# Kernel tuning notes

Measured on AMD Instinct MI355X. Metric: run time of the kernel, lower is better.

Reference implementation:

```python
import jax, jax.numpy as jnp
import numpy as np

B, S, DIM = 2, 2048, 2048
NH, NKV, HD = 32, 8, 64
N_REP = NH // NKV


def apply_rope(x, cos, sin):
    # x: (B, H, S, HD); cos/sin: (S, HD//2)
    d = x.shape[-1] // 2
    x1, x2 = x[..., :d], x[..., d:]
    c = cos[None, None, :, :]
    s = sin[None, None, :, :]
    return jnp.concatenate([x1 * c - x2 * s, x2 * c + x1 * s], axis=-1)


def setup_inputs() -> dict:
    key = jax.random.key(0)
    ks = jax.random.split(key, 8)
    x = jax.random.normal(ks[0], (B, S, DIM), dtype=jnp.float32)
    # plausible RoPE tables
    inv_freq = 1.0 / (10000.0 ** (jnp.arange(0, HD, 2, dtype=jnp.float32) / HD))
    t = jnp.arange(S, dtype=jnp.float32)
    freqs = jnp.outer(t, inv_freq)  # (S, HD//2)
    rope_cos = jnp.cos(freqs)
    rope_sin = jnp.sin(freqs)
    doc_ids = jnp.sort(jax.random.randint(ks[1], (B, S), 0, 8, dtype=jnp.int32), axis=-1)
    std = 0.02
    Wq = jax.random.normal(ks[2], (NH * HD, DIM), dtype=jnp.float32) * std
    Wk = jax.random.normal(ks[3], (NKV * HD, DIM), dtype=jnp.float32) * std
    Wv = jax.random.normal(ks[4], (NKV * HD, DIM), dtype=jnp.float32) * std
    Wo = jax.random.normal(ks[5], (DIM, NH * HD), dtype=jnp.float32) * std
    return {"x": x, "rope_cos": rope_cos, "rope_sin": rope_sin,
            "doc_ids": doc_ids, "Wq": Wq, "Wk": Wk, "Wv": Wv, "Wo": Wo}


def reference(x, rope_cos, rope_sin, doc_ids, Wq, Wk, Wv, Wo):
    batch, seq_len, _ = x.shape
    q = (x @ Wq.T).reshape(batch, seq_len, NH, HD).transpose(0, 2, 1, 3)   # (B,NH,S,HD)
    k = (x @ Wk.T).reshape(batch, seq_len, NKV, HD).transpose(0, 2, 1, 3)  # (B,NKV,S,HD)
    v = (x @ Wv.T).reshape(batch, seq_len, NKV, HD).transpose(0, 2, 1, 3)

    q = apply_rope(q, rope_cos, rope_sin)
    k = apply_rope(k, rope_cos, rope_sin)

    # GQA expansion (repeat_interleave on head dim)
    k = jnp.repeat(k, N_REP, axis=1)  # (B,NH,S,HD)
    v = jnp.repeat(v, N_REP, axis=1)

    # block-diagonal causal mask from packed doc ids
    doc_mask = doc_ids[:, :, None] == doc_ids[:, None, :]          # (B,S,S)
    causal = jnp.tril(jnp.ones((seq_len, seq_len), dtype=bool))    # (S,S)
    mask = (doc_mask & causal[None])[:, None, :, :]                # (B,1,S,S)

    scale = 1.0 / jnp.sqrt(jnp.asarray(HD, dtype=q.dtype))
    scores = jnp.einsum("bhqd,bhkd->bhqk", q, k) * scale
    scores = jnp.where(mask, scores, jnp.finfo(scores.dtype).min)
    attn = jax.nn.softmax(scores, axis=-1)
    out = jnp.einsum("bhqk,bhkd->bhqd", attn, v)                   # (B,NH,S,HD)
    out = out.transpose(0, 2, 1, 3).reshape(batch, seq_len, NH * HD)
    return out @ Wo.T
```

## Files before the change

### kernel.cpp

```cpp
#include <hip/hip_runtime.h>
#include <hip/hip_bf16.h>

#define BB   2
#define SEQ  2048
#define DIMD 2048
#define NHH  32
#define NKVV 8
#define HDD  64
#define QKVS 3072

typedef __bf16 bf16x8 __attribute__((ext_vector_type(8)));
typedef float  floatx4 __attribute__((ext_vector_type(4)));

typedef __attribute__((address_space(1))) const void* gas_ptr;
typedef __attribute__((address_space(3))) void*       las_ptr;

__device__ __forceinline__ unsigned short f2bu(float f) {
    __hip_bfloat16 h = __float2bfloat16(f);
    return *reinterpret_cast<unsigned short*>(&h);
}

#define C_X  (8u  * 1024 * 1024)
#define C_WQ (4u  * 1024 * 1024)
#define C_WK (1u  * 1024 * 1024)
#define C_WV (1u  * 1024 * 1024)
#define C_WO (4u  * 1024 * 1024)
__global__ void cvt_all(const float* __restrict__ x,  const float* __restrict__ wq,
                        const float* __restrict__ wk, const float* __restrict__ wv,
                        const float* __restrict__ wo,
                        __hip_bfloat16* __restrict__ xb,
                        __hip_bfloat16* __restrict__ wqkv,
                        __hip_bfloat16* __restrict__ wob)
{
    unsigned i = (blockIdx.x * blockDim.x + threadIdx.x) * 4;
    const float* src; __hip_bfloat16* dst;
    if (i < C_X)                       { src = x  + i;                    dst = xb + i; }
    else if (i < C_X + C_WQ)           { unsigned o = i - C_X;            src = wq + o; dst = wqkv + o; }
    else if (i < C_X + C_WQ + C_WK)    { unsigned o = i - C_X - C_WQ;     src = wk + o; dst = wqkv + C_WQ + o; }
    else if (i < C_X + C_WQ + C_WK + C_WV) { unsigned o = i - C_X - C_WQ - C_WK; src = wv + o; dst = wqkv + C_WQ + C_WK + o; }
    else                               { unsigned o = i - C_X - C_WQ - C_WK - C_WV; if (o >= C_WO) return; src = wo + o; dst = wob + o; }
    float4 v = *reinterpret_cast<const float4*>(src);
    dst[0] = __float2bfloat16(v.x);
    dst[1] = __float2bfloat16(v.y);
    dst[2] = __float2bfloat16(v.z);
    dst[3] = __float2bfloat16(v.w);
}

template <typename OutT, bool ROPE>
__global__ __launch_bounds__(256) void gemm_lds(
    const __hip_bfloat16* __restrict__ Abf,
    const __hip_bfloat16* __restrict__ Wbf,
    OutT* __restrict__ C,
    int M, int N, int K, int ldc,
    const float* __restrict__ cosb, const float* __restrict__ sinb)
{
    const __bf16* A = reinterpret_cast<const __bf16*>(Abf);
    const __bf16* W = reinterpret_cast<const __bf16*>(Wbf);

    __shared__ __bf16 As[128 * 32];
    __shared__ __bf16 Bs[128 * 32];

    int tid  = threadIdx.x;
    int wid  = tid >> 6;
    int lane = tid & 63;
    int l15  = lane & 15;
    int l4   = lane >> 4;
    int wm   = (wid & 1) * 64;
    int wn   = (wid >> 1) * 64;
    int bm   = blockIdx.x * 128;
    int bn   = blockIdx.y * 128;

    int r0 = tid >> 2,         g0 = (tid & 3) ^ ((r0 >> 1) & 3);
    int r1 = (tid + 256) >> 2, g1 = (tid & 3) ^ ((r1 >> 1) & 3);

    const __bf16* a0 = A + (size_t)(bm + r0) * K + g0 * 8;
    const __bf16* a1 = A + (size_t)(bm + r1) * K + g1 * 8;
    const __bf16* w0 = W + (size_t)(bn + r0) * K + g0 * 8;
    const __bf16* w1 = W + (size_t)(bn + r1) * K + g1 * 8;

    __bf16* lA0 = As + tid * 8;
    __bf16* lA1 = As + (tid + 256) * 8;
    __bf16* lB0 = Bs + tid * 8;
    __bf16* lB1 = Bs + (tid + 256) * 8;

    int arow[4], aslot[4], brow[4], bslot[4];
    #pragma unroll
    for (int i = 0; i < 4; ++i) {
        int ra = wm + i * 16 + l15;
        int rb = wn + i * 16 + l15;
        arow[i] = ra; aslot[i] = l4 ^ ((ra >> 1) & 3);
        brow[i] = rb; bslot[i] = l4 ^ ((rb >> 1) & 3);
    }

    floatx4 acc[4][4] = {};

    for (int k0 = 0; k0 < K; k0 += 32) {
        __builtin_amdgcn_global_load_lds((gas_ptr)(a0 + k0), (las_ptr)lA0, 16, 0, 0);
        __builtin_amdgcn_global_load_lds((gas_ptr)(a1 + k0), (las_ptr)lA1, 16, 0, 0);
        __builtin_amdgcn_global_load_lds((gas_ptr)(w0 + k0), (las_ptr)lB0, 16, 0, 0);
        __builtin_amdgcn_global_load_lds((gas_ptr)(w1 + k0), (las_ptr)lB1, 16, 0, 0);
        __syncthreads();

        bf16x8 af[4], bfr[4];
        #pragma unroll
        for (int i = 0; i < 4; ++i)
            af[i] = *reinterpret_cast<const bf16x8*>(As + arow[i] * 32 + aslot[i] * 8);
        #pragma unroll
        for (int j = 0; j < 4; ++j)
            bfr[j] = *reinterpret_cast<const bf16x8*>(Bs + brow[j] * 32 + bslot[j] * 8);

        #pragma unroll
        for (int i = 0; i < 4; ++i)
            #pragma unroll
            for (int j = 0; j < 4; ++j)
                acc[i][j] = __builtin_amdgcn_mfma_f32_16x16x32_bf16(af[i], bfr[j], acc[i][j], 0, 0, 0);
        __syncthreads();
    }

    if constexpr (ROPE) {
        bool do_rope = (bn + wn) < 2560;
        #pragma unroll
        for (int i = 0; i < 4; ++i) {
            #pragma unroll
            for (int r = 0; r < 4; ++r) {
                int row = bm + wm + i * 16 + l4 * 4 + r;
                int s   = row & (SEQ - 1);
                #pragma unroll
                for (int j = 0; j < 2; ++j) {
                    float x1 = acc[i][j][r], x2 = acc[i][j + 2][r];
                    if (do_rope) {
                        float cf = cosb[s * 32 + j * 16 + l15];
                        float sf = sinb[s * 32 + j * 16 + l15];
                        float o1 = x1 * cf - x2 * sf;
                        float o2 = x2 * cf + x1 * sf;
                        x1 = o1; x2 = o2;
                    }
                    int col = bn + wn + j * 16 + l15;
                    C[(size_t)row * ldc + col]      = __float2bfloat16(x1);
                    C[(size_t)row * ldc + col + 32] = __float2bfloat16(x2);
                }
            }
        }
    } else {
        #pragma unroll
        for (int i = 0; i < 4; ++i)
            #pragma unroll
            for (int j = 0; j < 4; ++j)
                #pragma unroll
                for (int r = 0; r < 4; ++r) {
                    int row = bm + wm + i * 16 + l4 * 4 + r;
                    int col = bn + wn + j * 16 + l15;
                    if constexpr (sizeof(OutT) == 4)
                        C[(size_t)row * ldc + col] = acc[i][j][r];
                    else
                        C[(size_t)row * ldc + col] = __float2bfloat16(acc[i][j][r]);
                }
    }
}

__global__ void transpose_v(const __hip_bfloat16* __restrict__ qkv,
                            unsigned short* __restrict__ vT)
{
    __shared__ unsigned short T[64][68];
    int s0  = blockIdx.x * 64;
    int kvh = blockIdx.y;
    int b   = blockIdx.z;
    int tid = threadIdx.x;

    int srow = tid >> 2, dg = (tid & 3) * 16;
    const unsigned short* src = reinterpret_cast<const unsigned short*>(qkv)
        + (size_t)(b * SEQ + s0 + srow) * QKVS + 2560 + kvh * 64 + dg;
    #pragma unroll
    for (int i = 0; i < 4; ++i)
        *reinterpret_cast<ushort4*>(&T[srow][dg + i * 4]) =
            *reinterpret_cast<const ushort4*>(src + i * 4);
    __syncthreads();

    int drow = tid >> 2, sg = (tid & 3) * 16;
    unsigned short* dst = vT + ((size_t)(b * NKVV + kvh) * 64 + drow) * SEQ + s0 + sg;
    #pragma unroll
    for (int i = 0; i < 4; ++i) {
        ushort4 u;
        u.x = T[sg + i * 4 + 0][drow];
        u.y = T[sg + i * 4 + 1][drow];
        u.z = T[sg + i * 4 + 2][drow];
        u.w = T[sg + i * 4 + 3][drow];
        *reinterpret_cast<ushort4*>(dst + i * 4) = u;
    }
}

__global__ __launch_bounds__(256) void attn_mfma(
    const __hip_bfloat16* __restrict__ qkv,
    const unsigned short* __restrict__ vT,
    const int* __restrict__ doc,
    __hip_bfloat16* __restrict__ ob)
{
    int qblk = (int)gridDim.x - 1 - (int)blockIdx.x;
    int h    = blockIdx.y;
    int b    = blockIdx.z;
    int kvh  = h >> 2;
    int tid  = threadIdx.x;
    int wv   = tid >> 6;
    int lane = tid & 63;
    int l15  = lane & 15;
    int l4   = lane >> 4;
    int q0   = qblk * 128;
    int qw   = q0 + wv * 32;

    __shared__ unsigned short Ks[64 * 64];
    __shared__ unsigned short Vts[64 * 64];
    __shared__ unsigned short Pb[4][32][76];
    __shared__ int kdoc[64];

    const unsigned short* qus = reinterpret_cast<const unsigned short*>(qkv);
    const unsigned short* kus = qus + 2048;

    bf16x8 aq[2][2];
    #pragma unroll
    for (int qt = 0; qt < 2; ++qt) {
        const unsigned short* qrow = qus + (size_t)(b * SEQ + qw + qt * 16 + l15) * QKVS + h * HDD;
        aq[qt][0] = *reinterpret_cast<const bf16x8*>(qrow + l4 * 8);
        aq[qt][1] = *reinterpret_cast<const bf16x8*>(qrow + 32 + l4 * 8);
    }
    int qd[2][4];
    #pragma unroll
    for (int qt = 0; qt < 2; ++qt)
        #pragma unroll
        for (int r = 0; r < 4; ++r)
            qd[qt][r] = doc[b * SEQ + qw + qt * 16 + l4 * 4 + r];
    int qd_w   = doc[b * SEQ + qw];
    int qd_blk = doc[b * SEQ + q0];

    float mrow[2][4], lrow[2][4];
    #pragma unroll
    for (int qt = 0; qt < 2; ++qt)
        #pragma unroll
        for (int r = 0; r < 4; ++r) { mrow[qt][r] = -1e30f; lrow[qt][r] = 0.f; }
    floatx4 accO[2][4] = {};

    int slot0 = tid, slot1 = tid + 256;
    int row0 = slot0 >> 3, g0 = (slot0 & 7) ^ (row0 & 7);
    int row1 = slot1 >> 3, g1 = (slot1 & 7) ^ (row1 & 7);
    const unsigned short* vtb = vT + ((size_t)(b * NKVV + kvh) * 64) * SEQ;

    int kc_end = 2 * qblk + 1;
    for (int kc = 0; kc <= kc_end; ++kc) {
        int k0 = kc * 64;
        int kd_last = doc[b * SEQ + k0 + 63];
        if (kd_last < qd_blk) continue;

        __syncthreads();
        __builtin_amdgcn_global_load_lds(
            (gas_ptr)(kus + (size_t)(b * SEQ + k0 + row0) * QKVS + kvh * HDD + g0 * 8),
            (las_ptr)(Ks + slot0 * 8), 16, 0, 0);
        __builtin_amdgcn_global_load_lds(
            (gas_ptr)(kus + (size_t)(b * SEQ + k0 + row1) * QKVS + kvh * HDD + g1 * 8),
            (las_ptr)(Ks + slot1 * 8), 16, 0, 0);
        __builtin_amdgcn_global_load_lds(
            (gas_ptr)(vtb + (size_t)row0 * SEQ + k0 + g0 * 8),
            (las_ptr)(Vts + slot0 * 8), 16, 0, 0);
        __builtin_amdgcn_global_load_lds(
            (gas_ptr)(vtb + (size_t)row1 * SEQ + k0 + g1 * 8),
            (las_ptr)(Vts + slot1 * 8), 16, 0, 0);
        if (tid < 64) kdoc[tid] = doc[b * SEQ + k0 + tid];
        __syncthreads();

        if (k0 <= qw + 31 && kd_last >= qd_w) {
            #pragma unroll
            for (int qt = 0; qt < 2; ++qt) {
                float s[4][4];
                #pragma unroll
                for (int t = 0; t < 4; ++t) {
                    int krow = t * 16 + l15;
                    bf16x8 bk0 = *reinterpret_cast<const bf16x8*>(Ks + krow * 64 + ((l4 ^ (krow & 7)) * 8));
                    bf16x8 bk1 = *reinterpret_cast<const bf16x8*>(Ks + krow * 64 + ((((l4 + 4)) ^ (krow & 7)) * 8));
                    floatx4 acc = {};
                    acc = __builtin_amdgcn_mfma_f32_16x16x32_bf16(aq[qt][0], bk0, acc, 0, 0, 0);
                    acc = __builtin_amdgcn_mfma_f32_16x16x32_bf16(aq[qt][1], bk1, acc, 0, 0, 0);
                    int key = k0 + krow;
                    int kd  = kdoc[krow];
                    #pragma unroll
                    for (int r = 0; r < 4; ++r) {
                        int qrow = qw + qt * 16 + l4 * 4 + r;
                        bool valid = (kd == qd[qt][r]) && (key <= qrow);
                        s[t][r] = valid ? acc[r] * 0.125f : -1e30f;
                    }
                }
                #pragma unroll
                for (int r = 0; r < 4; ++r) {
                    float pm = fmaxf(fmaxf(s[0][r], s[1][r]), fmaxf(s[2][r], s[3][r]));
                    pm = fmaxf(pm, __shfl_xor(pm, 1));
                    pm = fmaxf(pm, __shfl_xor(pm, 2));
                    pm = fmaxf(pm, __shfl_xor(pm, 4));
                    pm = fmaxf(pm, __shfl_xor(pm, 8));
                    float mnew = fmaxf(mrow[qt][r], pm);
                    float alpha = __expf(mrow[qt][r] - mnew);
                    mrow[qt][r] = mnew;
                    float ps = 0.f;
                    #pragma unroll
                    for (int t = 0; t < 4; ++t) {
                        float p = (s[t][r] <= -1e29f) ? 0.f : __expf(s[t][r] - mnew);
                        Pb[wv][qt * 16 + l4 * 4 + r][t * 16 + l15] = f2bu(p);
                        ps += p;
                    }
                    ps += __shfl_xor(ps, 1);
                    ps += __shfl_xor(ps, 2);
                    ps += __shfl_xor(ps, 4);
                    ps += __shfl_xor(ps, 8);
                    lrow[qt][r] = lrow[qt][r] * alpha + ps;
                    #pragma unroll
                    for (int t = 0; t < 4; ++t) accO[qt][t][r] *= alpha;
                }
            }
            #pragma unroll
            for (int qt = 0; qt < 2; ++qt) {
                bf16x8 ap0 = *reinterpret_cast<const bf16x8*>(&Pb[wv][qt * 16 + l15][l4 * 8]);
                bf16x8 ap1 = *reinterpret_cast<const bf16x8*>(&Pb[wv][qt * 16 + l15][32 + l4 * 8]);
                #pragma unroll
                for (int t = 0; t < 4; ++t) {
                    int vrow = t * 16 + l15;
                    bf16x8 bv0 = *reinterpret_cast<const bf16x8*>(Vts + vrow * 64 + ((l4 ^ (vrow & 7)) * 8));
                    bf16x8 bv1 = *reinterpret_cast<const bf16x8*>(Vts + vrow * 64 + ((((l4 + 4)) ^ (vrow & 7)) * 8));
                    accO[qt][t] = __builtin_amdgcn_mfma_f32_16x16x32_bf16(ap0, bv0, accO[qt][t], 0, 0, 0);
                    accO[qt][t] = __builtin_amdgcn_mfma_f32_16x16x32_bf16(ap1, bv1, accO[qt][t], 0, 0, 0);
                }
            }
        }
    }

    #pragma unroll
    for (int qt = 0; qt < 2; ++qt)
        #pragma unroll
        for (int r = 0; r < 4; ++r) {
            float inv = 1.0f / lrow[qt][r];
            size_t base = (size_t)(b * SEQ + qw + qt * 16 + l4 * 4 + r) * (NHH * HDD) + h * HDD;
            #pragma unroll
            for (int t = 0; t < 4; ++t)
                ob[base + t * 16 + l15] = __float2bfloat16(accO[qt][t][r] * inv);
        }
}

extern "C" void kernel_launch(void* const* d_in, const int* in_sizes, int n_in,
                              void* d_out, int out_size, void* d_ws, size_t ws_size,
                              hipStream_t stream) {
    const float* x  = (const float*)d_in[0];
    const float* rc = (const float*)d_in[1];
    const float* rs = (const float*)d_in[2];
    const int*   dc = (const int*)d_in[3];
    const float* Wq = (const float*)d_in[4];
    const float* Wk = (const float*)d_in[5];
    const float* Wv = (const float*)d_in[6];
    const float* Wo = (const float*)d_in[7];
    float* out = (float*)d_out;

    const int M   = BB * SEQ;
    const int KVD = NKVV * HDD;
    const int QKVN = DIMD + 2 * KVD;

    char* ws = (char*)d_ws;
    size_t off = 0;
    auto alloc = [&](size_t elems) { __hip_bfloat16* p = (__hip_bfloat16*)(ws + off); off += elems * 2; return p; };
    __hip_bfloat16* xb   = alloc((size_t)M * DIMD);
    __hip_bfloat16* wqkv = alloc((size_t)QKVN * DIMD);
    __hip_bfloat16* wob  = alloc((size_t)DIMD * DIMD);
    __hip_bfloat16* qkv  = alloc((size_t)M * QKVN);
    __hip_bfloat16* abuf = alloc((size_t)M * DIMD);
    unsigned short* vtb  = (unsigned short*)alloc((size_t)BB * NKVV * HDD * SEQ);

    {
        unsigned total4 = (C_X + C_WQ + C_WK + C_WV + C_WO) / 4;
        cvt_all<<<dim3((total4 + 255) / 256), 256, 0, stream>>>(
            x, Wq, Wk, Wv, Wo, xb, wqkv, wob);
    }

    gemm_lds<__hip_bfloat16, true><<<dim3(M / 128, QKVN / 128), 256, 0, stream>>>(
        xb, wqkv, qkv, M, QKVN, DIMD, QKVN, rc, rs);

    transpose_v<<<dim3(SEQ / 64, NKVV, BB), 256, 0, stream>>>(qkv, vtb);

    attn_mfma<<<dim3(SEQ / 128, NHH, BB), 256, 0, stream>>>(qkv, vtb, dc, abuf);

    gemm_lds<float, false><<<dim3(M / 128, DIMD / 128), 256, 0, stream>>>(
        abuf, wob, out, M, DIMD, DIMD, DIMD, nullptr, nullptr);
}
```

Baseline: 304.7 us.

## Replace GEMM with 8-wave double-buffered 256-row tile kernel with interleaved staging

Replaces the simple 128x128 single-buffer GEMM with a 512-thread kernel that computes 256xBN tiles (BN=256 for the QKV projection, 128 for the output projection), using K-tiles of 64 and double-buffered LDS. Global-to-LDS loads for the next tile are interleaved with MFMA phases, with explicit barriers, waitcnt and setprio. A remapped 1D grid groups workgroups for better cache locality. The aim is to hide memory latency and raise data reuse per tile. In exchange it uses much more LDS, fewer and larger workgroups, and fragile hand scheduling whose correctness depends on the waitcnt counts.

```diff
diff --git a/kernel.cpp b/kernel.cpp
--- a/kernel.cpp
+++ b/kernel.cpp
@@ -14,6 +14,9 @@
 
 typedef __attribute__((address_space(1))) const void* gas_ptr;
 typedef __attribute__((address_space(3))) void*       las_ptr;
+
+#define MFMA16 __builtin_amdgcn_mfma_f32_16x16x32_bf16
+#define CBAR() asm volatile("" ::: "memory")
 
 __device__ __forceinline__ unsigned short f2bu(float f) {
     __hip_bfloat16 h = __float2bfloat16(f);
@@ -46,88 +49,161 @@
     dst[3] = __float2bfloat16(v.w);
 }
 
-template <typename OutT, bool ROPE>
-__global__ __launch_bounds__(256) void gemm_lds(
+template <typename OutT, bool ROPE, int BN>
+__global__ __launch_bounds__(512, 2) void gemm8p(
     const __hip_bfloat16* __restrict__ Abf,
     const __hip_bfloat16* __restrict__ Wbf,
     OutT* __restrict__ C,
     int M, int N, int K, int ldc,
     const float* __restrict__ cosb, const float* __restrict__ sinb)
 {
-    const __bf16* A = reinterpret_cast<const __bf16*>(Abf);
-    const __bf16* W = reinterpret_cast<const __bf16*>(Wbf);
-
-    __shared__ __bf16 As[128 * 32];
-    __shared__ __bf16 Bs[128 * 32];
-
-    int tid  = threadIdx.x;
-    int wid  = tid >> 6;
-    int lane = tid & 63;
-    int l15  = lane & 15;
-    int l4   = lane >> 4;
-    int wm   = (wid & 1) * 64;
-    int wn   = (wid >> 1) * 64;
-    int bm   = blockIdx.x * 128;
-    int bn   = blockIdx.y * 128;
-
-    int r0 = tid >> 2,         g0 = (tid & 3) ^ ((r0 >> 1) & 3);
-    int r1 = (tid + 256) >> 2, g1 = (tid & 3) ^ ((r1 >> 1) & 3);
-
-    const __bf16* a0 = A + (size_t)(bm + r0) * K + g0 * 8;
-    const __bf16* a1 = A + (size_t)(bm + r1) * K + g1 * 8;
-    const __bf16* w0 = W + (size_t)(bn + r0) * K + g0 * 8;
-    const __bf16* w1 = W + (size_t)(bn + r1) * K + g1 * 8;
-
-    __bf16* lA0 = As + tid * 8;
-    __bf16* lA1 = As + (tid + 256) * 8;
-    __bf16* lB0 = Bs + tid * 8;
-    __bf16* lB1 = Bs + (tid + 256) * 8;
-
-    int arow[4], aslot[4], brow[4], bslot[4];
-    #pragma unroll
-    for (int i = 0; i < 4; ++i) {
-        int ra = wm + i * 16 + l15;
-        int rb = wn + i * 16 + l15;
-        arow[i] = ra; aslot[i] = l4 ^ ((ra >> 1) & 3);
-        brow[i] = rb; bslot[i] = l4 ^ ((rb >> 1) & 3);
-    }
-
-    floatx4 acc[4][4] = {};
-
-    for (int k0 = 0; k0 < K; k0 += 32) {
-        __builtin_amdgcn_global_load_lds((gas_ptr)(a0 + k0), (las_ptr)lA0, 16, 0, 0);
-        __builtin_amdgcn_global_load_lds((gas_ptr)(a1 + k0), (las_ptr)lA1, 16, 0, 0);
-        __builtin_amdgcn_global_load_lds((gas_ptr)(w0 + k0), (las_ptr)lB0, 16, 0, 0);
-        __builtin_amdgcn_global_load_lds((gas_ptr)(w1 + k0), (las_ptr)lB1, 16, 0, 0);
-        __syncthreads();
-
-        bf16x8 af[4], bfr[4];
-        #pragma unroll
-        for (int i = 0; i < 4; ++i)
-            af[i] = *reinterpret_cast<const bf16x8*>(As + arow[i] * 32 + aslot[i] * 8);
-        #pragma unroll
-        for (int j = 0; j < 4; ++j)
-            bfr[j] = *reinterpret_cast<const bf16x8*>(Bs + brow[j] * 32 + bslot[j] * 8);
-
-        #pragma unroll
-        for (int i = 0; i < 4; ++i)
-            #pragma unroll
-            for (int j = 0; j < 4; ++j)
-                acc[i][j] = __builtin_amdgcn_mfma_f32_16x16x32_bf16(af[i], bfr[j], acc[i][j], 0, 0, 0);
-        __syncthreads();
+    constexpr int  NF = BN / 64;
+    constexpr int  WN = BN / 4;
+    constexpr bool B2 = (BN == 256);
+    constexpr int  HB = (BN / 2) * 64;
+
+    const __bf16* Ag = reinterpret_cast<const __bf16*>(Abf);
+    const __bf16* Wg = reinterpret_cast<const __bf16*>(Wbf);
+
+    __shared__ __align__(16) __bf16 As[2][256 * 64];
+    __shared__ __align__(16) __bf16 Bs[2][BN * 64];
+
+    const int NT   = K >> 6;
+    const int tid  = threadIdx.x;
+    const int wid  = tid >> 6;
+    const int lane = tid & 63;
+    const int l15  = lane & 15;
+    const int l4   = lane >> 4;
+    const int wm   = wid >> 2;
+    const int wn   = wid & 3;
+
+    const int gx   = M >> 8;
+    const int nwg  = (int)gridDim.x;
+    const int orig = (int)blockIdx.x;
+    const int wg   = (orig & 7) * (nwg >> 3) + (orig >> 3);
+    const int bm   = (wg % gx) << 8;
+    const int bn   = (wg / gx) * BN;
+
+    const int r0 = tid >> 3;
+    const int c0 = ((tid & 7) ^ (r0 & 7)) * 8;
+    const __bf16* aS00 = Ag + (size_t)(bm + r0) * K + c0;
+    const __bf16* aS01 = aS00 + (size_t)64  * K;
+    const __bf16* aS10 = aS00 + (size_t)128 * K;
+    const __bf16* aS11 = aS00 + (size_t)192 * K;
+    const __bf16* bS00 = Wg + (size_t)(bn + r0) * K + c0;
+    const __bf16* bS01 = bS00 + (size_t)64 * K;
+    const __bf16* bS10 = bS00 + (size_t)(BN / 2) * K;
+    const __bf16* bS11 = bS10 + (size_t)64 * K;
+
+    bf16x8 af[4][2], b01[2][2], b23[2][2];
+    floatx4 acc[8][NF] = {};
+
+    auto stage2 = [&](const __bf16* s0, const __bf16* s1, __bf16* d, int kt) {
+        int k0 = (kt < NT ? kt : NT - 1) << 6;
+        __builtin_amdgcn_global_load_lds((gas_ptr)(s0 + k0), (las_ptr)(d + tid * 8), 16, 0, 0);
+        if (s1)
+        __builtin_amdgcn_global_load_lds((gas_ptr)(s1 + k0), (las_ptr)(d + 4096 + tid * 8), 16, 0, 0);
+    };
+    auto lda = [&](int buf, int mbase) {
+        #pragma unroll
+        for (int mi = 0; mi < 4; ++mi)
+            #pragma unroll
+            for (int kk = 0; kk < 2; ++kk) {
+                int row = wm * 128 + (mbase + mi) * 16 + l15;
+                int ch  = ((kk * 4 + l4) ^ (row & 7)) * 8;
+                af[mi][kk] = *reinterpret_cast<const bf16x8*>(&As[buf][row * 64 + ch]);
+            }
+    };
+    auto ldb = [&](int buf, bf16x8 (&regs)[2][2], int nbase) {
+        #pragma unroll
+        for (int ni = 0; ni < 2; ++ni)
+            #pragma unroll
+            for (int kk = 0; kk < 2; ++kk) {
+                int row = wn * WN + (nbase + ni) * 16 + l15;
+                int ch  = ((kk * 4 + l4) ^ (row & 7)) * 8;
+                regs[ni][kk] = *reinterpret_cast<const bf16x8*>(&Bs[buf][row * 64 + ch]);
+            }
+    };
+    auto mmBoth = [&](int mbase, bf16x8 (&bregs)[2][2], int nb) {
+        #pragma unroll
+        for (int mi = 0; mi < 4; ++mi)
+            #pragma unroll
+            for (int ni = 0; ni < 2; ++ni) {
+                acc[mbase + mi][nb + ni] = MFMA16(af[mi][0], bregs[ni][0], acc[mbase + mi][nb + ni], 0, 0, 0);
+                acc[mbase + mi][nb + ni] = MFMA16(af[mi][1], bregs[ni][1], acc[mbase + mi][nb + ni], 0, 0, 0);
+            }
+    };
+    auto mmOne = [&](int mbase, int kk) {
+        #pragma unroll
+        for (int mi = 0; mi < 4; ++mi)
+            #pragma unroll
+            for (int ni = 0; ni < 2; ++ni)
+                acc[mbase + mi][ni] = MFMA16(af[mi][kk], b01[ni][kk], acc[mbase + mi][ni], 0, 0, 0);
+    };
+
+    auto ktile = [&](int cur, int t) {
+        lda(cur, 0);
+        ldb(cur, b01, 0);
+        stage2(aS10, aS11, &As[cur ^ 1][8192], t + 1);
+        CBAR(); __builtin_amdgcn_s_barrier(); CBAR();
+        asm volatile("s_waitcnt lgkmcnt(0)" ::: "memory");
+        __builtin_amdgcn_sched_barrier(0);
+        __builtin_amdgcn_s_setprio(1);
+        if constexpr (B2) mmBoth(0, b01, 0); else mmOne(0, 0);
+        __builtin_amdgcn_s_setprio(0);
+        CBAR(); __builtin_amdgcn_s_barrier(); CBAR();
+        if constexpr (B2) ldb(cur, b23, 2);
+        stage2(bS00, B2 ? bS01 : (const __bf16*)nullptr, &Bs[cur ^ 1][0], t + 1);
+        CBAR(); __builtin_amdgcn_s_barrier(); CBAR();
+        asm volatile("s_waitcnt lgkmcnt(0)" ::: "memory");
+        __builtin_amdgcn_sched_barrier(0);
+        __builtin_amdgcn_s_setprio(1);
+        if constexpr (B2) mmBoth(0, b23, 2); else mmOne(0, 1);
+        __builtin_amdgcn_s_setprio(0);
+        CBAR(); __builtin_amdgcn_s_barrier(); CBAR();
+        lda(cur, 4);
+        stage2(bS10, B2 ? bS11 : (const __bf16*)nullptr, &Bs[cur ^ 1][HB], t + 1);
+        CBAR(); __builtin_amdgcn_s_barrier(); CBAR();
+        asm volatile("s_waitcnt lgkmcnt(0)" ::: "memory");
+        __builtin_amdgcn_sched_barrier(0);
+        __builtin_amdgcn_s_setprio(1);
+        if constexpr (B2) mmBoth(4, b23, 2); else mmOne(4, 1);
+        __builtin_amdgcn_s_setprio(0);
+        CBAR(); __builtin_amdgcn_s_barrier(); CBAR();
+        stage2(aS00, aS01, &As[cur][0], t + 2);
+        CBAR(); __builtin_amdgcn_s_barrier(); CBAR();
+        __builtin_amdgcn_s_setprio(1);
+        if constexpr (B2) mmBoth(4, b01, 0); else mmOne(4, 0);
+        __builtin_amdgcn_s_setprio(0);
+        asm volatile("s_waitcnt vmcnt(2)" ::: "memory");
+        CBAR(); __builtin_amdgcn_s_barrier(); CBAR();
+    };
+
+    stage2(aS00, aS01, &As[0][0],    0);
+    stage2(aS10, aS11, &As[0][8192], 0);
+    stage2(bS00, B2 ? bS01 : (const __bf16*)nullptr, &Bs[0][0],  0);
+    stage2(bS10, B2 ? bS11 : (const __bf16*)nullptr, &Bs[0][HB], 0);
+    stage2(aS00, aS01, &As[1][0],    1);
+    asm volatile("s_waitcnt vmcnt(2)" ::: "memory");
+    CBAR(); __builtin_amdgcn_s_barrier(); CBAR();
+
+    #pragma unroll 1
+    for (int t = 0; t < NT; t += 2) {
+        ktile(0, t);
+        ktile(1, t + 1);
     }
 
     if constexpr (ROPE) {
-        bool do_rope = (bn + wn) < 2560;
-        #pragma unroll
-        for (int i = 0; i < 4; ++i) {
+        bool do_rope = (bn + wn * 64) < 2560;
+        #pragma unroll
+        for (int mi = 0; mi < 8; ++mi) {
             #pragma unroll
             for (int r = 0; r < 4; ++r) {
-                int row = bm + wm + i * 16 + l4 * 4 + r;
+                int row = bm + wm * 128 + mi * 16 + l4 * 4 + r;
                 int s   = row & (SEQ - 1);
                 #pragma unroll
                 for (int j = 0; j < 2; ++j) {
-                    float x1 = acc[i][j][r], x2 = acc[i][j + 2][r];
+                    float x1 = acc[mi][j][r], x2 = acc[mi][j + 2][r];
                     if (do_rope) {
                         float cf = cosb[s * 32 + j * 16 + l15];
                         float sf = sinb[s * 32 + j * 16 + l15];
@@ -135,7 +211,7 @@
                         float o2 = x2 * cf + x1 * sf;
                         x1 = o1; x2 = o2;
                     }
-                    int col = bn + wn + j * 16 + l15;
+                    int col = bn + wn * 64 + j * 16 + l15;
                     C[(size_t)row * ldc + col]      = __float2bfloat16(x1);
                     C[(size_t)row * ldc + col + 32] = __float2bfloat16(x2);
                 }
@@ -143,17 +219,17 @@
         }
     } else {
         #pragma unroll
-        for (int i = 0; i < 4; ++i)
-            #pragma unroll
-            for (int j = 0; j < 4; ++j)
+        for (int mi = 0; mi < 8; ++mi)
+            #pragma unroll
+            for (int ni = 0; ni < NF; ++ni)
                 #pragma unroll
                 for (int r = 0; r < 4; ++r) {
-                    int row = bm + wm + i * 16 + l4 * 4 + r;
-                    int col = bn + wn + j * 16 + l15;
+                    int row = bm + wm * 128 + mi * 16 + l4 * 4 + r;
+                    int col = bn + wn * WN + ni * 16 + l15;
                     if constexpr (sizeof(OutT) == 4)
-                        C[(size_t)row * ldc + col] = acc[i][j][r];
+                        C[(size_t)row * ldc + col] = acc[mi][ni][r];
                     else
-                        C[(size_t)row * ldc + col] = __float2bfloat16(acc[i][j][r]);
+                        C[(size_t)row * ldc + col] = __float2bfloat16(acc[mi][ni][r]);
                 }
     }
 }
@@ -275,8 +351,8 @@
                     bf16x8 bk0 = *reinterpret_cast<const bf16x8*>(Ks + krow * 64 + ((l4 ^ (krow & 7)) * 8));
                     bf16x8 bk1 = *reinterpret_cast<const bf16x8*>(Ks + krow * 64 + ((((l4 + 4)) ^ (krow & 7)) * 8));
                     floatx4 acc = {};
-                    acc = __builtin_amdgcn_mfma_f32_16x16x32_bf16(aq[qt][0], bk0, acc, 0, 0, 0);
-                    acc = __builtin_amdgcn_mfma_f32_16x16x32_bf16(aq[qt][1], bk1, acc, 0, 0, 0);
+                    acc = MFMA16(aq[qt][0], bk0, acc, 0, 0, 0);
+                    acc = MFMA16(aq[qt][1], bk1, acc, 0, 0, 0);
                     int key = k0 + krow;
                     int kd  = kdoc[krow];
                     #pragma unroll
@@ -321,8 +397,8 @@
                     int vrow = t * 16 + l15;
                     bf16x8 bv0 = *reinterpret_cast<const bf16x8*>(Vts + vrow * 64 + ((l4 ^ (vrow & 7)) * 8));
                     bf16x8 bv1 = *reinterpret_cast<const bf16x8*>(Vts + vrow * 64 + ((((l4 + 4)) ^ (vrow & 7)) * 8));
-                    accO[qt][t] = __builtin_amdgcn_mfma_f32_16x16x32_bf16(ap0, bv0, accO[qt][t], 0, 0, 0);
-                    accO[qt][t] = __builtin_amdgcn_mfma_f32_16x16x32_bf16(ap1, bv1, accO[qt][t], 0, 0, 0);
+                    accO[qt][t] = MFMA16(ap0, bv0, accO[qt][t], 0, 0, 0);
+                    accO[qt][t] = MFMA16(ap1, bv1, accO[qt][t], 0, 0, 0);
                 }
             }
         }
@@ -353,8 +429,8 @@
     const float* Wo = (const float*)d_in[7];
     float* out = (float*)d_out;
 
-    const int M   = BB * SEQ;
-    const int KVD = NKVV * HDD;
+    const int M    = BB * SEQ;
+    const int KVD  = NKVV * HDD;
     const int QKVN = DIMD + 2 * KVD;
 
     char* ws = (char*)d_ws;
@@ -373,13 +449,13 @@
             x, Wq, Wk, Wv, Wo, xb, wqkv, wob);
     }
 
-    gemm_lds<__hip_bfloat16, true><<<dim3(M / 128, QKVN / 128), 256, 0, stream>>>(
+    gemm8p<__hip_bfloat16, true, 256><<<dim3((M / 256) * (QKVN / 256)), 512, 0, stream>>>(
         xb, wqkv, qkv, M, QKVN, DIMD, QKVN, rc, rs);
 
     transpose_v<<<dim3(SEQ / 64, NKVV, BB), 256, 0, stream>>>(qkv, vtb);
 
     attn_mfma<<<dim3(SEQ / 128, NHH, BB), 256, 0, stream>>>(qkv, vtb, dc, abuf);
 
-    gemm_lds<float, false><<<dim3(M / 128, DIMD / 128), 256, 0, stream>>>(
+    gemm8p<float, false, 128><<<dim3((M / 256) * (DIMD / 128)), 512, 0, stream>>>(
         abuf, wob, out, M, DIMD, DIMD, DIMD, nullptr, nullptr);
 }
```

Result: faster. 298.3 us (-2.1%).

## Fuse V transpose into QKV GEMM epilogue and double-buffer attention K/V tiles

Applied to the files above, without the earlier changes.

The QKV GEMM epilogue now writes V columns straight into the transposed V layout, which removes the separate transpose kernel and its extra read and write of V. The attention kernel precomputes a ballot mask of key chunks that can be relevant for the block, then double-buffers the K, V and doc-id tiles in LDS so the next chunk's loads overlap the current chunk's compute. Doc ids are also staged asynchronously. The risks are more LDS use, which may lower occupancy, and the correctness of the hand-written vmcnt waits.

```diff
diff --git a/kernel.cpp b/kernel.cpp
--- a/kernel.cpp
+++ b/kernel.cpp
@@ -14,6 +14,9 @@
 
 typedef __attribute__((address_space(1))) const void* gas_ptr;
 typedef __attribute__((address_space(3))) void*       las_ptr;
+
+#define MFMA16 __builtin_amdgcn_mfma_f32_16x16x32_bf16
+#define CBAR() asm volatile("" ::: "memory")
 
 __device__ __forceinline__ unsigned short f2bu(float f) {
     __hip_bfloat16 h = __float2bfloat16(f);
@@ -52,7 +55,8 @@
     const __hip_bfloat16* __restrict__ Wbf,
     OutT* __restrict__ C,
     int M, int N, int K, int ldc,
-    const float* __restrict__ cosb, const float* __restrict__ sinb)
+    const float* __restrict__ cosb, const float* __restrict__ sinb,
+    unsigned short* __restrict__ vT)
 {
     const __bf16* A = reinterpret_cast<const __bf16*>(Abf);
     const __bf16* W = reinterpret_cast<const __bf16*>(Wbf);
@@ -113,31 +117,47 @@
         for (int i = 0; i < 4; ++i)
             #pragma unroll
             for (int j = 0; j < 4; ++j)
-                acc[i][j] = __builtin_amdgcn_mfma_f32_16x16x32_bf16(af[i], bfr[j], acc[i][j], 0, 0, 0);
+                acc[i][j] = MFMA16(af[i], bfr[j], acc[i][j], 0, 0, 0);
         __syncthreads();
     }
 
+    const int col0 = bn + wn;
     if constexpr (ROPE) {
-        bool do_rope = (bn + wn) < 2560;
-        #pragma unroll
-        for (int i = 0; i < 4; ++i) {
-            #pragma unroll
-            for (int r = 0; r < 4; ++r) {
-                int row = bm + wm + i * 16 + l4 * 4 + r;
-                int s   = row & (SEQ - 1);
-                #pragma unroll
-                for (int j = 0; j < 2; ++j) {
-                    float x1 = acc[i][j][r], x2 = acc[i][j + 2][r];
-                    if (do_rope) {
+        if (col0 >= 2560) {
+            int kvh = (col0 - 2560) >> 6;
+            int b   = bm >> 11;
+            int s0  = (bm & (SEQ - 1)) + wm + l4 * 4;
+            #pragma unroll
+            for (int i = 0; i < 4; ++i)
+                #pragma unroll
+                for (int ni = 0; ni < 4; ++ni) {
+                    int d = ni * 16 + l15;
+                    ushort4 u;
+                    u.x = f2bu(acc[i][ni][0]);
+                    u.y = f2bu(acc[i][ni][1]);
+                    u.z = f2bu(acc[i][ni][2]);
+                    u.w = f2bu(acc[i][ni][3]);
+                    *reinterpret_cast<ushort4*>(
+                        vT + ((size_t)(b * NKVV + kvh) * 64 + d) * SEQ + s0 + i * 16) = u;
+                }
+        } else {
+            #pragma unroll
+            for (int i = 0; i < 4; ++i) {
+                #pragma unroll
+                for (int r = 0; r < 4; ++r) {
+                    int row = bm + wm + i * 16 + l4 * 4 + r;
+                    int s   = row & (SEQ - 1);
+                    #pragma unroll
+                    for (int j = 0; j < 2; ++j) {
+                        float x1 = acc[i][j][r], x2 = acc[i][j + 2][r];
                         float cf = cosb[s * 32 + j * 16 + l15];
                         float sf = sinb[s * 32 + j * 16 + l15];
                         float o1 = x1 * cf - x2 * sf;
                         float o2 = x2 * cf + x1 * sf;
-                        x1 = o1; x2 = o2;
+                        int col = col0 + j * 16 + l15;
+                        C[(size_t)row * ldc + col]      = __float2bfloat16(o1);
+                        C[(size_t)row * ldc + col + 32] = __float2bfloat16(o2);
                     }
-                    int col = bn + wn + j * 16 + l15;
-                    C[(size_t)row * ldc + col]      = __float2bfloat16(x1);
-                    C[(size_t)row * ldc + col + 32] = __float2bfloat16(x2);
                 }
             }
         }
@@ -149,43 +169,12 @@
                 #pragma unroll
                 for (int r = 0; r < 4; ++r) {
                     int row = bm + wm + i * 16 + l4 * 4 + r;
-                    int col = bn + wn + j * 16 + l15;
+                    int col = col0 + j * 16 + l15;
                     if constexpr (sizeof(OutT) == 4)
                         C[(size_t)row * ldc + col] = acc[i][j][r];
                     else
                         C[(size_t)row * ldc + col] = __float2bfloat16(acc[i][j][r]);
                 }
-    }
-}
-
-__global__ void transpose_v(const __hip_bfloat16* __restrict__ qkv,
-                            unsigned short* __restrict__ vT)
-{
-    __shared__ unsigned short T[64][68];
-    int s0  = blockIdx.x * 64;
-    int kvh = blockIdx.y;
-    int b   = blockIdx.z;
-    int tid = threadIdx.x;
-
-    int srow = tid >> 2, dg = (tid & 3) * 16;
-    const unsigned short* src = reinterpret_cast<const unsigned short*>(qkv)
-        + (size_t)(b * SEQ + s0 + srow) * QKVS + 2560 + kvh * 64 + dg;
-    #pragma unroll
-    for (int i = 0; i < 4; ++i)
-        *reinterpret_cast<ushort4*>(&T[srow][dg + i * 4]) =
-            *reinterpret_cast<const ushort4*>(src + i * 4);
-    __syncthreads();
-
-    int drow = tid >> 2, sg = (tid & 3) * 16;
-    unsigned short* dst = vT + ((size_t)(b * NKVV + kvh) * 64 + drow) * SEQ + s0 + sg;
-    #pragma unroll
-    for (int i = 0; i < 4; ++i) {
-        ushort4 u;
-        u.x = T[sg + i * 4 + 0][drow];
-        u.y = T[sg + i * 4 + 1][drow];
-        u.z = T[sg + i * 4 + 2][drow];
-        u.w = T[sg + i * 4 + 3][drow];
-        *reinterpret_cast<ushort4*>(dst + i * 4) = u;
     }
 }
 
@@ -207,13 +196,14 @@
     int q0   = qblk * 128;
     int qw   = q0 + wv * 32;
 
-    __shared__ unsigned short Ks[64 * 64];
-    __shared__ unsigned short Vts[64 * 64];
+    __shared__ unsigned short Ks[2][64 * 64];
+    __shared__ unsigned short Vts[2][64 * 64];
+    __shared__ int            kdoc[2][64];
     __shared__ unsigned short Pb[4][32][76];
-    __shared__ int kdoc[64];
 
     const unsigned short* qus = reinterpret_cast<const unsigned short*>(qkv);
     const unsigned short* kus = qus + 2048;
+    const int* docb = doc + b * SEQ;
 
     bf16x8 aq[2][2];
     #pragma unroll
@@ -227,9 +217,9 @@
     for (int qt = 0; qt < 2; ++qt)
         #pragma unroll
         for (int r = 0; r < 4; ++r)
-            qd[qt][r] = doc[b * SEQ + qw + qt * 16 + l4 * 4 + r];
-    int qd_w   = doc[b * SEQ + qw];
-    int qd_blk = doc[b * SEQ + q0];
+            qd[qt][r] = docb[qw + qt * 16 + l4 * 4 + r];
+    int qd_w   = docb[qw];
+    int qd_blk = docb[q0];
 
     float mrow[2][4], lrow[2][4];
     #pragma unroll
@@ -244,27 +234,52 @@
     const unsigned short* vtb = vT + ((size_t)(b * NKVV + kvh) * 64) * SEQ;
 
     int kc_end = 2 * qblk + 1;
-    for (int kc = 0; kc <= kc_end; ++kc) {
+    unsigned mask;
+    {
+        bool v = false;
+        if (lane <= kc_end && lane < 32)
+            v = (docb[lane * 64 + 63] >= qd_blk);
+        mask = (unsigned)__ballot(v);
+    }
+
+    auto stagec = [&](int buf, int kc) {
         int k0 = kc * 64;
-        int kd_last = doc[b * SEQ + k0 + 63];
-        if (kd_last < qd_blk) continue;
-
-        __syncthreads();
         __builtin_amdgcn_global_load_lds(
             (gas_ptr)(kus + (size_t)(b * SEQ + k0 + row0) * QKVS + kvh * HDD + g0 * 8),
-            (las_ptr)(Ks + slot0 * 8), 16, 0, 0);
+            (las_ptr)(&Ks[buf][slot0 * 8]), 16, 0, 0);
         __builtin_amdgcn_global_load_lds(
             (gas_ptr)(kus + (size_t)(b * SEQ + k0 + row1) * QKVS + kvh * HDD + g1 * 8),
-            (las_ptr)(Ks + slot1 * 8), 16, 0, 0);
+            (las_ptr)(&Ks[buf][slot1 * 8]), 16, 0, 0);
         __builtin_amdgcn_global_load_lds(
             (gas_ptr)(vtb + (size_t)row0 * SEQ + k0 + g0 * 8),
-            (las_ptr)(Vts + slot0 * 8), 16, 0, 0);
+            (las_ptr)(&Vts[buf][slot0 * 8]), 16, 0, 0);
         __builtin_amdgcn_global_load_lds(
             (gas_ptr)(vtb + (size_t)row1 * SEQ + k0 + g1 * 8),
-            (las_ptr)(Vts + slot1 * 8), 16, 0, 0);
-        if (tid < 64) kdoc[tid] = doc[b * SEQ + k0 + tid];
-        __syncthreads();
-
+            (las_ptr)(&Vts[buf][slot1 * 8]), 16, 0, 0);
+        __builtin_amdgcn_global_load_lds(
+            (gas_ptr)(docb + k0 + lane),
+            (las_ptr)(&kdoc[buf][lane]), 4, 0, 0);
+    };
+
+    int p  = 0;
+    int kc = (int)__builtin_ctz(mask);
+    mask &= mask - 1;
+    stagec(0, kc);
+
+    while (true) {
+        int nkc = -1;
+        if (mask) {
+            nkc = (int)__builtin_ctz(mask);
+            mask &= mask - 1;
+            stagec(p ^ 1, nkc);
+            asm volatile("s_waitcnt vmcnt(5)" ::: "memory");
+        } else {
+            asm volatile("s_waitcnt vmcnt(0)" ::: "memory");
+        }
+        CBAR(); __builtin_amdgcn_s_barrier(); CBAR();
+
+        int k0 = kc * 64;
+        int kd_last = kdoc[p][63];
         if (k0 <= qw + 31 && kd_last >= qd_w) {
             #pragma unroll
             for (int qt = 0; qt < 2; ++qt) {
@@ -272,13 +287,13 @@
                 #pragma unroll
                 for (int t = 0; t < 4; ++t) {
                     int krow = t * 16 + l15;
-                    bf16x8 bk0 = *reinterpret_cast<const bf16x8*>(Ks + krow * 64 + ((l4 ^ (krow & 7)) * 8));
-                    bf16x8 bk1 = *reinterpret_cast<const bf16x8*>(Ks + krow * 64 + ((((l4 + 4)) ^ (krow & 7)) * 8));
+                    bf16x8 bk0 = *reinterpret_cast<const bf16x8*>(&Ks[p][krow * 64 + ((l4 ^ (krow & 7)) * 8)]);
+                    bf16x8 bk1 = *reinterpret_cast<const bf16x8*>(&Ks[p][krow * 64 + ((((l4 + 4)) ^ (krow & 7)) * 8)]);
                     floatx4 acc = {};
-                    acc = __builtin_amdgcn_mfma_f32_16x16x32_bf16(aq[qt][0], bk0, acc, 0, 0, 0);
-                    acc = __builtin_amdgcn_mfma_f32_16x16x32_bf16(aq[qt][1], bk1, acc, 0, 0, 0);
+                    acc = MFMA16(aq[qt][0], bk0, acc, 0, 0, 0);
+                    acc = MFMA16(aq[qt][1], bk1, acc, 0, 0, 0);
                     int key = k0 + krow;
-                    int kd  = kdoc[krow];
+                    int kd  = kdoc[p][krow];
                     #pragma unroll
                     for (int r = 0; r < 4; ++r) {
                         int qrow = qw + qt * 16 + l4 * 4 + r;
@@ -299,9 +314,9 @@
                     float ps = 0.f;
                     #pragma unroll
                     for (int t = 0; t < 4; ++t) {
-                        float p = (s[t][r] <= -1e29f) ? 0.f : __expf(s[t][r] - mnew);
-                        Pb[wv][qt * 16 + l4 * 4 + r][t * 16 + l15] = f2bu(p);
-                        ps += p;
+                        float pv = (s[t][r] <= -1e29f) ? 0.f : __expf(s[t][r] - mnew);
+                        Pb[wv][qt * 16 + l4 * 4 + r][t * 16 + l15] = f2bu(pv);
+                        ps += pv;
                     }
                     ps += __shfl_xor(ps, 1);
                     ps += __shfl_xor(ps, 2);
@@ -319,13 +334,16 @@
                 #pragma unroll
                 for (int t = 0; t < 4; ++t) {
                     int vrow = t * 16 + l15;
-                    bf16x8 bv0 = *reinterpret_cast<const bf16x8*>(Vts + vrow * 64 + ((l4 ^ (vrow & 7)) * 8));
-                    bf16x8 bv1 = *reinterpret_cast<const bf16x8*>(Vts + vrow * 64 + ((((l4 + 4)) ^ (vrow & 7)) * 8));
-                    accO[qt][t] = __builtin_amdgcn_mfma_f32_16x16x32_bf16(ap0, bv0, accO[qt][t], 0, 0, 0);
-                    accO[qt][t] = __builtin_amdgcn_mfma_f32_16x16x32_bf16(ap1, bv1, accO[qt][t], 0, 0, 0);
+                    bf16x8 bv0 = *reinterpret_cast<const bf16x8*>(&Vts[p][vrow * 64 + ((l4 ^ (vrow & 7)) * 8)]);
+                    bf16x8 bv1 = *reinterpret_cast<const bf16x8*>(&Vts[p][vrow * 64 + ((((l4 + 4)) ^ (vrow & 7)) * 8)]);
+                    accO[qt][t] = MFMA16(ap0, bv0, accO[qt][t], 0, 0, 0);
+                    accO[qt][t] = MFMA16(ap1, bv1, accO[qt][t], 0, 0, 0);
                 }
             }
         }
+        CBAR(); __builtin_amdgcn_s_barrier(); CBAR();
+        if (nkc < 0) break;
+        kc = nkc; p ^= 1;
     }
 
     #pragma unroll
@@ -353,8 +371,8 @@
     const float* Wo = (const float*)d_in[7];
     float* out = (float*)d_out;
 
-    const int M   = BB * SEQ;
-    const int KVD = NKVV * HDD;
+    const int M    = BB * SEQ;
+    const int KVD  = NKVV * HDD;
     const int QKVN = DIMD + 2 * KVD;
 
     char* ws = (char*)d_ws;
@@ -374,12 +392,10 @@
     }
 
     gemm_lds<__hip_bfloat16, true><<<dim3(M / 128, QKVN / 128), 256, 0, stream>>>(
-        xb, wqkv, qkv, M, QKVN, DIMD, QKVN, rc, rs);
-
-    transpose_v<<<dim3(SEQ / 64, NKVV, BB), 256, 0, stream>>>(qkv, vtb);
+        xb, wqkv, qkv, M, QKVN, DIMD, QKVN, rc, rs, vtb);
 
     attn_mfma<<<dim3(SEQ / 128, NHH, BB), 256, 0, stream>>>(qkv, vtb, dc, abuf);
 
     gemm_lds<float, false><<<dim3(M / 128, DIMD / 128), 256, 0, stream>>>(
-        abuf, wob, out, M, DIMD, DIMD, DIMD, nullptr, nullptr);
+        abuf, wob, out, M, DIMD, DIMD, DIMD, nullptr, nullptr, nullptr);
 }
```

New measurement: 278.3 us. 8.6% less time.
